# Kernel tuning notes

Measured on AMD Instinct MI355X. Metric: run time of the kernel, lower is better.

## Reference

```python
import jax, jax.numpy as jnp
import numpy as np

TEMPERATURE_F = 0.5
FEATURE_DIM = 1024
CLASS_NUM = 8192


def setup_inputs() -> dict:
    key = jax.random.key(0)
    k1, k2 = jax.random.split(key)
    h_i = jax.random.normal(k1, (FEATURE_DIM, CLASS_NUM), dtype=jnp.float32)
    h_j = jax.random.normal(k2, (FEATURE_DIM, CLASS_NUM), dtype=jnp.float32)
    return {"h_i": h_i, "h_j": h_j}


def reference(h_i, h_j):
    # memory_Loss.forward_modal (NT-Xent over class prototypes)
    C = h_i.shape[1]
    N = 2 * C
    h = jnp.concatenate([h_i, h_j], axis=1)          # [D, N]
    sim = jnp.matmul(h.T, h) / TEMPERATURE_F          # [N, N]
    idx = jnp.arange(N)
    partner = (idx + C) % N                           # positive-pair index per row
    pos = sim[idx, partner]                           # [N] = diag(sim, +C) ++ diag(sim, -C)
    # mask_correlated_samples: drop diagonal and the +/-C partner entry
    mask = (idx[None, :] != idx[:, None]) & (idx[None, :] != partner[:, None])
    neg = jnp.where(mask, sim, -jnp.inf)              # [N, N], N-2 finite per row
    # CrossEntropy(logits=[pos, negs], label=0) = -pos + logsumexp([pos, negs])
    lse = jnp.logaddexp(pos, jax.scipy.special.logsumexp(neg, axis=1))
    loss = jnp.sum(lse - pos) / N
    return loss
```

## Files before the change

### kernel.cpp

```cpp
#include <hip/hip_runtime.h>
#include <stdint.h>

#define FD 1024
#define NC 8192
#define NT 16384
#define NKT 16

typedef __attribute__((ext_vector_type(8))) short bf16x8;
typedef __attribute__((ext_vector_type(4))) float f32x4;

__device__ __forceinline__ unsigned short f2bf(float f) {
  unsigned u = __float_as_uint(f);
  u += 0x7FFF + ((u >> 16) & 1);
  return (unsigned short)(u >> 16);
}
__device__ __forceinline__ float bf2f(unsigned short s) {
  return __uint_as_float(((unsigned)s) << 16);
}

__device__ __forceinline__ void gld16(const void* g, void* l) {
  __builtin_amdgcn_global_load_lds(
      (const __attribute__((address_space(1))) unsigned int*)g,
      (__attribute__((address_space(3))) unsigned int*)l, 16, 0, 0);
}

__device__ __forceinline__ void cas_merge(unsigned long long* p, float m2, float s2) {
  unsigned long long old = *p, assumed;
  do {
    assumed = old;
    float m1 = __uint_as_float((unsigned)(assumed & 0xffffffffull));
    float s1 = __uint_as_float((unsigned)(assumed >> 32));
    float mn = fmaxf(m1, m2);
    float s = s1 * __expf(m1 - mn) + s2 * __expf(m2 - mn);
    unsigned long long nv =
        ((unsigned long long)__float_as_uint(s) << 32) | __float_as_uint(mn);
    old = atomicCAS(p, assumed, nv);
  } while (old != assumed);
}

__device__ __forceinline__ void decode_tile(int xcd, int p, int& ti, int& tj) {
  if (p < 20) {
    const int hi = (p >= 10) ? 1 : 0;
    const int d = 2 * xcd + hi;
    const int q = p - hi * 10;
    int i = 0;
    while ((i + 1) * 4 - ((i + 1) * i) / 2 <= q) ++i;
    const int j = i + (q - (i * 4 - (i * (i - 1)) / 2));
    ti = d * 4 + i; tj = d * 4 + j;
  } else {
    const int t = p - 20;
    const int o = 15 * xcd + (t >> 4);
    const int q = t & 15;
    int SI = 0;
    while (15 * (SI + 1) - ((SI + 1) * SI) / 2 <= o) ++SI;
    const int SJ = SI + 1 + (o - (15 * SI - (SI * (SI - 1)) / 2));
    ti = SI * 4 + (q >> 2); tj = SJ * 4 + (q & 3);
  }
}

__global__ void nt_xent_init(unsigned long long* __restrict__ G) {
  G[blockIdx.x * 256 + threadIdx.x] = 0xFF800000ull;
}

__global__ void nt_xent_transpose(const float* __restrict__ hi,
                                  const float* __restrict__ hj,
                                  unsigned short* __restrict__ HT) {
  __shared__ unsigned short tile[64][65];
  const int bn = blockIdx.x, bd = blockIdx.y;
  const int n0 = bn * 64, d0 = bd * 64;
  const float* src = (n0 < NC) ? hi : hj;
  const int nb = (n0 < NC) ? n0 : n0 - NC;
  const int tid = threadIdx.x;
#pragma unroll
  for (int i = 0; i < 16; ++i) {
    int idx = tid + 256 * i;
    int dl = idx >> 6, nl = idx & 63;
    float f = src[(size_t)(d0 + dl) * NC + nb + nl];
    tile[nl][dl] = f2bf(f);
  }
  __syncthreads();
#pragma unroll
  for (int i = 0; i < 16; ++i) {
    int idx = tid + 256 * i;
    int nl = idx >> 6, dl = idx & 63;
    HT[(size_t)(n0 + nl) * FD + d0 + dl] = tile[nl][dl];
  }
}

__global__ __launch_bounds__(512, 1)
void nt_xent_gemm_lse(const unsigned short* __restrict__ HT,
                      unsigned long long* __restrict__ G) {
  __shared__ __align__(16) unsigned char lds[143360];

  const int tid = threadIdx.x;
  const int w = tid >> 6, l = tid & 63;
  const int lr = l & 15;
  const int lk = (l >> 4) * 8;
  const int wr = w >> 2, wc = w & 3;

  const int xcd = blockIdx.x & 7;
  const int slot = blockIdx.x >> 3;

#define STAGE2(AB, BB, KO, DBUF, KK, ISB) do {                               \
    const unsigned short* _s = (ISB) ? (BB) : (AB);                          \
    unsigned char* _d = lds + (DBUF) * 65536 + (ISB) * 32768 +               \
                        (KK) * 16384 + (2 * w) * 1024;                       \
    const int _ko = (KO) + (KK) * 32 + lk;                                   \
    gld16(_s + (((size_t)(2 * w * 16 + lr)) << 10) + _ko, _d);               \
    gld16(_s + (((size_t)((2 * w + 1) * 16 + lr)) << 10) + _ko, _d + 1024);  \
  } while (0)

#define RDA(BUF, KK, MI) \
  (*(const bf16x8*)(lds + (BUF) * 65536 + (KK) * 16384 + (wr * 8 + (MI)) * 1024 + l * 16))
#define RDB(BUF, KK, N) \
  (*(const bf16x8*)(lds + (BUF) * 65536 + 32768 + (KK) * 16384 + (wc * 4 + (N)) * 1024 + l * 16))

#define MFMA16(MB)                                                           \
  _Pragma("unroll") for (int m = 0; m < 4; ++m)                              \
  _Pragma("unroll") for (int n = 0; n < 4; ++n)                              \
    acc[(MB) + m][n] = __builtin_amdgcn_mfma_f32_16x16x32_bf16(              \
        av[m], bv[n], acc[(MB) + m][n], 0, 0, 0);

#define VM4 asm volatile("s_waitcnt vmcnt(4)" ::: "memory")

#define KTILE(BUF, NA, NB, NKO) do {                                         \
    bv[0] = RDB(BUF, 0, 0); bv[1] = RDB(BUF, 0, 1);                          \
    bv[2] = RDB(BUF, 0, 2); bv[3] = RDB(BUF, 0, 3);                          \
    av[0] = RDA(BUF, 0, 0); av[1] = RDA(BUF, 0, 1);                          \
    av[2] = RDA(BUF, 0, 2); av[3] = RDA(BUF, 0, 3);                          \
    STAGE2(NA, NB, NKO, (BUF) ^ 1, 0, 0);                                    \
    __builtin_amdgcn_s_barrier();                                            \
    __builtin_amdgcn_s_setprio(1); MFMA16(0) __builtin_amdgcn_s_setprio(0);  \
    __builtin_amdgcn_s_barrier();                                            \
    av[0] = RDA(BUF, 0, 4); av[1] = RDA(BUF, 0, 5);                          \
    av[2] = RDA(BUF, 0, 6); av[3] = RDA(BUF, 0, 7);                          \
    STAGE2(NA, NB, NKO, (BUF) ^ 1, 0, 1);                                    \
    VM4;                                                                     \
    __builtin_amdgcn_s_barrier();                                            \
    __builtin_amdgcn_s_setprio(1); MFMA16(4) __builtin_amdgcn_s_setprio(0);  \
    __builtin_amdgcn_s_barrier();                                            \
    bv[0] = RDB(BUF, 1, 0); bv[1] = RDB(BUF, 1, 1);                          \
    bv[2] = RDB(BUF, 1, 2); bv[3] = RDB(BUF, 1, 3);                          \
    av[0] = RDA(BUF, 1, 0); av[1] = RDA(BUF, 1, 1);                          \
    av[2] = RDA(BUF, 1, 2); av[3] = RDA(BUF, 1, 3);                          \
    STAGE2(NA, NB, NKO, (BUF) ^ 1, 1, 0);                                    \
    __builtin_amdgcn_s_barrier();                                            \
    __builtin_amdgcn_s_setprio(1); MFMA16(0) __builtin_amdgcn_s_setprio(0);  \
    __builtin_amdgcn_s_barrier();                                            \
    av[0] = RDA(BUF, 1, 4); av[1] = RDA(BUF, 1, 5);                          \
    av[2] = RDA(BUF, 1, 6); av[3] = RDA(BUF, 1, 7);                          \
    STAGE2(NA, NB, NKO, (BUF) ^ 1, 1, 1);                                    \
    VM4;                                                                     \
    __builtin_amdgcn_s_barrier();                                            \
    __builtin_amdgcn_s_setprio(1); MFMA16(4) __builtin_amdgcn_s_setprio(0);  \
    __builtin_amdgcn_s_barrier();                                            \
  } while (0)

  f32x4 acc[8][4];
#pragma unroll
  for (int a = 0; a < 8; ++a)
#pragma unroll
    for (int b = 0; b < 4; ++b) acc[a][b] = (f32x4){0.f, 0.f, 0.f, 0.f};
  bf16x8 av[4], bv[4];

  int p = slot, ti, tj;
  decode_tile(xcd, p, ti, tj);
  const unsigned short* Acur = HT + (((size_t)ti) << 18);
  const unsigned short* Bcur = HT + (((size_t)tj) << 18);
  STAGE2(Acur, Bcur, 0, 0, 0, 0);
  STAGE2(Acur, Bcur, 0, 0, 0, 1);
  STAGE2(Acur, Bcur, 0, 0, 1, 0);
  STAGE2(Acur, Bcur, 0, 0, 1, 1);
  asm volatile("s_waitcnt vmcnt(0)" ::: "memory");
  __builtin_amdgcn_s_barrier();

  while (true) {
    const int pn = p + 32;
    const bool has_next = (pn < 260);
    int tin = 0, tjn = 0;
    if (has_next) decode_tile(xcd, pn, tin, tjn);
    const unsigned short* Anx = HT + (((size_t)tin) << 18);
    const unsigned short* Bnx = HT + (((size_t)tjn) << 18);

#pragma unroll 1
    for (int Tp = 0; Tp < 7; ++Tp) {
      KTILE(0, Acur, Bcur, (2 * Tp + 1) * 64);
      KTILE(1, Acur, Bcur, (2 * Tp + 2) * 64);
    }
    KTILE(0, Acur, Bcur, 15 * 64);
    KTILE(1, Anx, Bnx, 0);

    {
      float (*red)[4][128][2] = (float (*)[4][128][2])(lds + 131072);
      float (*redc)[2][64][2] = (float (*)[2][64][2])(lds + 139264);
      const int gr0 = ti * 256 + wr * 128 + ((l >> 4) << 2);
      const int gc0 = tj * 256 + wc * 64 + lr;
#pragma unroll
      for (int m = 0; m < 8; ++m) {
#pragma unroll
        for (int rg = 0; rg < 4; ++rg) {
          const int grow = gr0 + m * 16 + rg;
          float vs[4];
          float mx = -INFINITY;
#pragma unroll
          for (int n = 0; n < 4; ++n) {
            float v = acc[m][n][rg] * 2.0f;
            if (gc0 + n * 16 == grow) v = -INFINITY;
            vs[n] = v;
            mx = fmaxf(mx, v);
          }
#pragma unroll
          for (int off = 1; off < 16; off <<= 1) mx = fmaxf(mx, __shfl_xor(mx, off, 16));
          float sm = 0.f;
#pragma unroll
          for (int n = 0; n < 4; ++n) sm += __expf(vs[n] - mx);
#pragma unroll
          for (int off = 1; off < 16; off <<= 1) sm += __shfl_xor(sm, off, 16);
          if (lr == 0) {
            const int rl = m * 16 + ((l >> 4) << 2) + rg;
            red[wr][wc][rl][0] = mx;
            red[wr][wc][rl][1] = sm;
          }
        }
      }
      if (ti != tj) {
#pragma unroll
        for (int n = 0; n < 4; ++n) {
          float mx = -INFINITY;
#pragma unroll
          for (int m = 0; m < 8; ++m)
#pragma unroll
            for (int rg = 0; rg < 4; ++rg) mx = fmaxf(mx, acc[m][n][rg] * 2.0f);
          mx = fmaxf(mx, __shfl_xor(mx, 16));
          mx = fmaxf(mx, __shfl_xor(mx, 32));
          float sm = 0.f;
#pragma unroll
          for (int m = 0; m < 8; ++m)
#pragma unroll
            for (int rg = 0; rg < 4; ++rg) sm += __expf(acc[m][n][rg] * 2.0f - mx);
          sm += __shfl_xor(sm, 16);
          sm += __shfl_xor(sm, 32);
          if (l < 16) {
            redc[wc][wr][n * 16 + lr][0] = mx;
            redc[wc][wr][n * 16 + lr][1] = sm;
          }
        }
      }
#pragma unroll
      for (int a = 0; a < 8; ++a)
#pragma unroll
        for (int b = 0; b < 4; ++b) acc[a][b] = (f32x4){0.f, 0.f, 0.f, 0.f};

      asm volatile("s_waitcnt lgkmcnt(0)" ::: "memory");
      __builtin_amdgcn_s_barrier();

      if (tid < 256) {
        const int row = tid, wrr = row >> 7, rl = row & 127;
        float M = -INFINITY;
#pragma unroll
        for (int c = 0; c < 4; ++c) M = fmaxf(M, red[wrr][c][rl][0]);
        float S = 0.f;
#pragma unroll
        for (int c = 0; c < 4; ++c) S += red[wrr][c][rl][1] * __expf(red[wrr][c][rl][0] - M);
        cas_merge(&G[ti * 256 + row], M, S);
      } else if (ti != tj) {
        const int col = tid - 256, wcc = col >> 6, cl = col & 63;
        float m0 = redc[wcc][0][cl][0], s0 = redc[wcc][0][cl][1];
        float m1 = redc[wcc][1][cl][0], s1 = redc[wcc][1][cl][1];
        float mn = fmaxf(m0, m1);
        float s = s0 * __expf(m0 - mn) + s1 * __expf(m1 - mn);
        cas_merge(&G[tj * 256 + col], mn, s);
      }
      __builtin_amdgcn_s_barrier();
    }

    if (!has_next) break;
    p = pn; ti = tin; tj = tjn; Acur = Anx; Bcur = Bnx;
  }

#undef STAGE2
#undef RDA
#undef RDB
#undef MFMA16
#undef VM4
#undef KTILE
}

__global__ void nt_xent_final(const unsigned short* __restrict__ HT,
                              const unsigned long long* __restrict__ G,
                              float* __restrict__ out) {
  const int tid = threadIdx.x;
  const int w = tid >> 6, l = tid & 63;
  const int wave = blockIdx.x * 4 + w;
  float local = 0.f;
  for (int rr = 0; rr < 16; ++rr) {
    int i = wave * 16 + rr;
    int p = (i + NC) & (NT - 1);
    const int4* A = (const int4*)(HT + (((size_t)i) << 10) + (l << 4));
    const int4* B = (const int4*)(HT + (((size_t)p) << 10) + (l << 4));
    union { int4 v; unsigned short u[8]; } a0, a1, b0, b1;
    a0.v = A[0]; a1.v = A[1]; b0.v = B[0]; b1.v = B[1];
    float dot = 0.f;
#pragma unroll
    for (int j = 0; j < 8; ++j) dot += bf2f(a0.u[j]) * bf2f(b0.u[j]);
#pragma unroll
    for (int j = 0; j < 8; ++j) dot += bf2f(a1.u[j]) * bf2f(b1.u[j]);
#pragma unroll
    for (int off = 1; off < 64; off <<= 1) dot += __shfl_xor(dot, off, 64);
    if (l == 0) {
      unsigned long long g = G[i];
      float m = __uint_as_float((unsigned)(g & 0xffffffffull));
      float s = __uint_as_float((unsigned)(g >> 32));
      local += m + __logf(s) - 2.0f * dot;
    }
  }
  if (l == 0) atomicAdd(out, local * (1.0f / (float)NT));
}

extern "C" void kernel_launch(void* const* d_in, const int* in_sizes, int n_in,
                              void* d_out, int out_size, void* d_ws, size_t ws_size,
                              hipStream_t stream) {
  const float* hi = (const float*)d_in[0];
  const float* hj = (const float*)d_in[1];
  unsigned short* HT = (unsigned short*)d_ws;
  unsigned long long* G = (unsigned long long*)((char*)d_ws + (size_t)NT * FD * 2);
  float* out = (float*)d_out;

  const size_t need = (size_t)NT * FD * 2 + (size_t)NT * 8;
  if (ws_size < need) return;

  hipMemsetAsync(out, 0, sizeof(float), stream);
  nt_xent_init<<<NT / 256, 256, 0, stream>>>(G);
  nt_xent_transpose<<<dim3(NT / 64, FD / 64), 256, 0, stream>>>(hi, hj, HT);
  nt_xent_gemm_lse<<<256, 512, 0, stream>>>(HT, G);
  nt_xent_final<<<NT / 64, 256, 0, stream>>>(HT, G, out);
}
```

Measured before the change: 530.6 us.

## Switch GEMM main loop to 32x32x16 bf16 MFMA with matching LDS layout

Replaces the 16x16x32 MFMA tiling with 32x32x16 MFMA instructions, changing the per-wave accumulator layout to 4x2 f32x16 tiles. The LDS staging layout, fragment reads and pipeline phases are restructured to fit, going from four phases per k-tile to two with fewer barriers. The fused row and column logsumexp epilogue is rewritten for the 32-lane row layout. The goal is to cut LDS reads and barrier overhead per FLOP, at the risk of a different register-pressure and scheduling balance.

```diff
diff --git a/kernel.cpp b/kernel.cpp
--- a/kernel.cpp
+++ b/kernel.cpp
@@ -4,10 +4,9 @@
 #define FD 1024
 #define NC 8192
 #define NT 16384
-#define NKT 16
 
 typedef __attribute__((ext_vector_type(8))) short bf16x8;
-typedef __attribute__((ext_vector_type(4))) float f32x4;
+typedef __attribute__((ext_vector_type(16))) float f32x16;
 
 __device__ __forceinline__ unsigned short f2bf(float f) {
   unsigned u = __float_as_uint(f);
@@ -94,83 +93,76 @@
 
   const int tid = threadIdx.x;
   const int w = tid >> 6, l = tid & 63;
-  const int lr = l & 15;
-  const int lk = (l >> 4) * 8;
+  const int lrow = l & 31;
+  const int lko = (l >> 5) * 8;
   const int wr = w >> 2, wc = w & 3;
+  const int hi5 = l >> 5;
 
   const int xcd = blockIdx.x & 7;
   const int slot = blockIdx.x >> 3;
 
-#define STAGE2(AB, BB, KO, DBUF, KK, ISB) do {                               \
-    const unsigned short* _s = (ISB) ? (BB) : (AB);                          \
+#define STAGEG(SRC, KO, DBUF, KK32, ISB) do {                                \
+    const unsigned short* _s = (SRC);                                        \
     unsigned char* _d = lds + (DBUF) * 65536 + (ISB) * 32768 +               \
-                        (KK) * 16384 + (2 * w) * 1024;                       \
-    const int _ko = (KO) + (KK) * 32 + lk;                                   \
-    gld16(_s + (((size_t)(2 * w * 16 + lr)) << 10) + _ko, _d);               \
-    gld16(_s + (((size_t)((2 * w + 1) * 16 + lr)) << 10) + _ko, _d + 1024);  \
+                        (KK32) * 16384 + w * 1024;                           \
+    const size_t _r = ((size_t)(w * 32 + lrow)) << 10;                       \
+    const int _kb = (KO) + (KK32) * 32 + lko;                                \
+    gld16(_s + _r + _kb, _d);                                                \
+    gld16(_s + _r + _kb + 16, _d + 8192);                                    \
   } while (0)
 
-#define RDA(BUF, KK, MI) \
-  (*(const bf16x8*)(lds + (BUF) * 65536 + (KK) * 16384 + (wr * 8 + (MI)) * 1024 + l * 16))
-#define RDB(BUF, KK, N) \
-  (*(const bf16x8*)(lds + (BUF) * 65536 + 32768 + (KK) * 16384 + (wc * 4 + (N)) * 1024 + l * 16))
-
-#define MFMA16(MB)                                                           \
-  _Pragma("unroll") for (int m = 0; m < 4; ++m)                              \
-  _Pragma("unroll") for (int n = 0; n < 4; ++n)                              \
-    acc[(MB) + m][n] = __builtin_amdgcn_mfma_f32_16x16x32_bf16(              \
-        av[m], bv[n], acc[(MB) + m][n], 0, 0, 0);
-
-#define VM4 asm volatile("s_waitcnt vmcnt(4)" ::: "memory")
-
-#define KTILE(BUF, NA, NB, NKO) do {                                         \
-    bv[0] = RDB(BUF, 0, 0); bv[1] = RDB(BUF, 0, 1);                          \
-    bv[2] = RDB(BUF, 0, 2); bv[3] = RDB(BUF, 0, 3);                          \
-    av[0] = RDA(BUF, 0, 0); av[1] = RDA(BUF, 0, 1);                          \
-    av[2] = RDA(BUF, 0, 2); av[3] = RDA(BUF, 0, 3);                          \
-    STAGE2(NA, NB, NKO, (BUF) ^ 1, 0, 0);                                    \
+#define RDA(BUF, KK32, K16H, MFi) \
+  (*(const bf16x8*)(lds + (BUF) * 65536 + (KK32) * 16384 + ((K16H) * 8 + wr * 4 + (MFi)) * 1024 + l * 16))
+#define RDB(BUF, KK32, K16H, NFi) \
+  (*(const bf16x8*)(lds + (BUF) * 65536 + 32768 + (KK32) * 16384 + ((K16H) * 8 + wc * 2 + (NFi)) * 1024 + l * 16))
+
+#define MFm(A, B, C) __builtin_amdgcn_mfma_f32_32x32x16_bf16(A, B, C, 0, 0, 0)
+
+#define PH(BUF, KK32, NA, NB, NKO) do {                                      \
+    bf16x8 a0 = RDA(BUF, KK32, 0, 0), a1 = RDA(BUF, KK32, 0, 1);             \
+    bf16x8 a2 = RDA(BUF, KK32, 0, 2), a3 = RDA(BUF, KK32, 0, 3);             \
+    bf16x8 a4 = RDA(BUF, KK32, 1, 0), a5 = RDA(BUF, KK32, 1, 1);             \
+    bf16x8 a6 = RDA(BUF, KK32, 1, 2), a7 = RDA(BUF, KK32, 1, 3);             \
+    bf16x8 b0 = RDB(BUF, KK32, 0, 0), b1 = RDB(BUF, KK32, 0, 1);             \
+    bf16x8 b2 = RDB(BUF, KK32, 1, 0), b3 = RDB(BUF, KK32, 1, 1);             \
+    STAGEG(NA, NKO, (BUF) ^ 1, KK32, 0);                                     \
+    STAGEG(NB, NKO, (BUF) ^ 1, KK32, 1);                                     \
+    asm volatile("s_waitcnt vmcnt(4)" ::: "memory");                         \
     __builtin_amdgcn_s_barrier();                                            \
-    __builtin_amdgcn_s_setprio(1); MFMA16(0) __builtin_amdgcn_s_setprio(0);  \
-    __builtin_amdgcn_s_barrier();                                            \
-    av[0] = RDA(BUF, 0, 4); av[1] = RDA(BUF, 0, 5);                          \
-    av[2] = RDA(BUF, 0, 6); av[3] = RDA(BUF, 0, 7);                          \
-    STAGE2(NA, NB, NKO, (BUF) ^ 1, 0, 1);                                    \
-    VM4;                                                                     \
-    __builtin_amdgcn_s_barrier();                                            \
-    __builtin_amdgcn_s_setprio(1); MFMA16(4) __builtin_amdgcn_s_setprio(0);  \
-    __builtin_amdgcn_s_barrier();                                            \
-    bv[0] = RDB(BUF, 1, 0); bv[1] = RDB(BUF, 1, 1);                          \
-    bv[2] = RDB(BUF, 1, 2); bv[3] = RDB(BUF, 1, 3);                          \
-    av[0] = RDA(BUF, 1, 0); av[1] = RDA(BUF, 1, 1);                          \
-    av[2] = RDA(BUF, 1, 2); av[3] = RDA(BUF, 1, 3);                          \
-    STAGE2(NA, NB, NKO, (BUF) ^ 1, 1, 0);                                    \
-    __builtin_amdgcn_s_barrier();                                            \
-    __builtin_amdgcn_s_setprio(1); MFMA16(0) __builtin_amdgcn_s_setprio(0);  \
-    __builtin_amdgcn_s_barrier();                                            \
-    av[0] = RDA(BUF, 1, 4); av[1] = RDA(BUF, 1, 5);                          \
-    av[2] = RDA(BUF, 1, 6); av[3] = RDA(BUF, 1, 7);                          \
-    STAGE2(NA, NB, NKO, (BUF) ^ 1, 1, 1);                                    \
-    VM4;                                                                     \
-    __builtin_amdgcn_s_barrier();                                            \
-    __builtin_amdgcn_s_setprio(1); MFMA16(4) __builtin_amdgcn_s_setprio(0);  \
+    __builtin_amdgcn_s_setprio(1);                                           \
+    acc[0][0] = MFm(a0, b0, acc[0][0]); acc[0][1] = MFm(a0, b1, acc[0][1]);  \
+    acc[1][0] = MFm(a1, b0, acc[1][0]); acc[1][1] = MFm(a1, b1, acc[1][1]);  \
+    acc[2][0] = MFm(a2, b0, acc[2][0]); acc[2][1] = MFm(a2, b1, acc[2][1]);  \
+    acc[3][0] = MFm(a3, b0, acc[3][0]); acc[3][1] = MFm(a3, b1, acc[3][1]);  \
+    acc[0][0] = MFm(a4, b2, acc[0][0]); acc[0][1] = MFm(a4, b3, acc[0][1]);  \
+    acc[1][0] = MFm(a5, b2, acc[1][0]); acc[1][1] = MFm(a5, b3, acc[1][1]);  \
+    acc[2][0] = MFm(a6, b2, acc[2][0]); acc[2][1] = MFm(a6, b3, acc[2][1]);  \
+    acc[3][0] = MFm(a7, b2, acc[3][0]); acc[3][1] = MFm(a7, b3, acc[3][1]);  \
+    __builtin_amdgcn_s_setprio(0);                                           \
     __builtin_amdgcn_s_barrier();                                            \
   } while (0)
 
-  f32x4 acc[8][4];
-#pragma unroll
-  for (int a = 0; a < 8; ++a)
-#pragma unroll
-    for (int b = 0; b < 4; ++b) acc[a][b] = (f32x4){0.f, 0.f, 0.f, 0.f};
-  bf16x8 av[4], bv[4];
+#define KTILE(BUF, NA, NB, NKO) do { \
+    PH(BUF, 0, NA, NB, NKO);         \
+    PH(BUF, 1, NA, NB, NKO);         \
+  } while (0)
+
+  f32x16 acc[4][2];
+#pragma unroll
+  for (int a = 0; a < 4; ++a)
+#pragma unroll
+    for (int b = 0; b < 2; ++b)
+#pragma unroll
+      for (int r = 0; r < 16; ++r) acc[a][b][r] = 0.f;
 
   int p = slot, ti, tj;
   decode_tile(xcd, p, ti, tj);
   const unsigned short* Acur = HT + (((size_t)ti) << 18);
   const unsigned short* Bcur = HT + (((size_t)tj) << 18);
-  STAGE2(Acur, Bcur, 0, 0, 0, 0);
-  STAGE2(Acur, Bcur, 0, 0, 0, 1);
-  STAGE2(Acur, Bcur, 0, 0, 1, 0);
-  STAGE2(Acur, Bcur, 0, 0, 1, 1);
+  STAGEG(Acur, 0, 0, 0, 0);
+  STAGEG(Bcur, 0, 0, 0, 1);
+  STAGEG(Acur, 0, 0, 1, 0);
+  STAGEG(Bcur, 0, 0, 1, 1);
   asm volatile("s_waitcnt vmcnt(0)" ::: "memory");
   __builtin_amdgcn_s_barrier();
 
@@ -193,31 +185,26 @@
     {
       float (*red)[4][128][2] = (float (*)[4][128][2])(lds + 131072);
       float (*redc)[2][64][2] = (float (*)[2][64][2])(lds + 139264);
-      const int gr0 = ti * 256 + wr * 128 + ((l >> 4) << 2);
-      const int gc0 = tj * 256 + wc * 64 + lr;
-#pragma unroll
-      for (int m = 0; m < 8; ++m) {
-#pragma unroll
-        for (int rg = 0; rg < 4; ++rg) {
-          const int grow = gr0 + m * 16 + rg;
-          float vs[4];
-          float mx = -INFINITY;
-#pragma unroll
-          for (int n = 0; n < 4; ++n) {
-            float v = acc[m][n][rg] * 2.0f;
-            if (gc0 + n * 16 == grow) v = -INFINITY;
-            vs[n] = v;
-            mx = fmaxf(mx, v);
-          }
-#pragma unroll
-          for (int off = 1; off < 16; off <<= 1) mx = fmaxf(mx, __shfl_xor(mx, off, 16));
-          float sm = 0.f;
-#pragma unroll
-          for (int n = 0; n < 4; ++n) sm += __expf(vs[n] - mx);
-#pragma unroll
-          for (int off = 1; off < 16; off <<= 1) sm += __shfl_xor(sm, off, 16);
-          if (lr == 0) {
-            const int rl = m * 16 + ((l >> 4) << 2) + rg;
+      const int gcn0 = tj * 256 + wc * 64 + lrow;
+#pragma unroll
+      for (int mf = 0; mf < 4; ++mf) {
+#pragma unroll
+        for (int r = 0; r < 16; ++r) {
+          const int rl = mf * 32 + (r & 3) + 8 * (r >> 2) + 4 * hi5;
+          const int grow = ti * 256 + wr * 128 + rl;
+          float v0 = acc[mf][0][r] * 2.0f;
+          float v1 = acc[mf][1][r] * 2.0f;
+          if (gcn0 == grow)      v0 = -INFINITY;
+          if (gcn0 + 32 == grow) v1 = -INFINITY;
+          float mx = fmaxf(v0, v1);
+#pragma unroll
+          for (int off = 1; off < 32; off <<= 1)
+            mx = fmaxf(mx, __shfl_xor(mx, off, 32));
+          float sm = __expf(v0 - mx) + __expf(v1 - mx);
+#pragma unroll
+          for (int off = 1; off < 32; off <<= 1)
+            sm += __shfl_xor(sm, off, 32);
+          if (lrow == 0) {
             red[wr][wc][rl][0] = mx;
             red[wr][wc][rl][1] = sm;
           }
@@ -225,31 +212,31 @@
       }
       if (ti != tj) {
 #pragma unroll
-        for (int n = 0; n < 4; ++n) {
+        for (int nf = 0; nf < 2; ++nf) {
           float mx = -INFINITY;
 #pragma unroll
-          for (int m = 0; m < 8; ++m)
-#pragma unroll
-            for (int rg = 0; rg < 4; ++rg) mx = fmaxf(mx, acc[m][n][rg] * 2.0f);
-          mx = fmaxf(mx, __shfl_xor(mx, 16));
+          for (int mf = 0; mf < 4; ++mf)
+#pragma unroll
+            for (int r = 0; r < 16; ++r) mx = fmaxf(mx, acc[mf][nf][r] * 2.0f);
           mx = fmaxf(mx, __shfl_xor(mx, 32));
           float sm = 0.f;
 #pragma unroll
-          for (int m = 0; m < 8; ++m)
-#pragma unroll
-            for (int rg = 0; rg < 4; ++rg) sm += __expf(acc[m][n][rg] * 2.0f - mx);
-          sm += __shfl_xor(sm, 16);
+          for (int mf = 0; mf < 4; ++mf)
+#pragma unroll
+            for (int r = 0; r < 16; ++r) sm += __expf(acc[mf][nf][r] * 2.0f - mx);
           sm += __shfl_xor(sm, 32);
-          if (l < 16) {
-            redc[wc][wr][n * 16 + lr][0] = mx;
-            redc[wc][wr][n * 16 + lr][1] = sm;
+          if (l < 32) {
+            redc[wc][wr][nf * 32 + lrow][0] = mx;
+            redc[wc][wr][nf * 32 + lrow][1] = sm;
           }
         }
       }
 #pragma unroll
-      for (int a = 0; a < 8; ++a)
-#pragma unroll
-        for (int b = 0; b < 4; ++b) acc[a][b] = (f32x4){0.f, 0.f, 0.f, 0.f};
+      for (int a = 0; a < 4; ++a)
+#pragma unroll
+        for (int b = 0; b < 2; ++b)
+#pragma unroll
+          for (int r = 0; r < 16; ++r) acc[a][b][r] = 0.f;
 
       asm volatile("s_waitcnt lgkmcnt(0)" ::: "memory");
       __builtin_amdgcn_s_barrier();
@@ -278,11 +265,11 @@
     p = pn; ti = tin; tj = tjn; Acur = Anx; Bcur = Bnx;
   }
 
-#undef STAGE2
+#undef STAGEG
 #undef RDA
 #undef RDB
-#undef MFMA16
-#undef VM4
+#undef MFm
+#undef PH
 #undef KTILE
 }
 
```

After: 670.1 us. +26.3%, slower.
